# Kernel optimization log

Hardware: AMD Instinct MI355X
Metric: run time of the kernel (lower is better)

## Reference

```python
import jax, jax.numpy as jnp
import numpy as np

NQ = 10          # num_qubits
NL = 4           # num_layers (StronglyEntanglingLayers)
DIM = 2 ** NQ    # state-vector dimension = input_linear out features
B = 4096
SEQ = 512
PRED = 96

# ---- static basis-state bookkeeping (wire 0 = most significant bit, as in PennyLane) ----

def _cnot_perm(control, target):
    s = np.arange(DIM)
    bit = (s >> (NQ - 1 - control)) & 1
    return s ^ (bit << (NQ - 1 - target))

def _layer_perms():
    # StronglyEntanglingLayers default ranges: r_l = (l % (n_wires - 1)) + 1,
    # then CNOT(i, (i+r) % n) for i = 0..n-1, applied sequentially.
    perms = []
    for l in range(NL):
        r = (l % (NQ - 1)) + 1
        comp = np.arange(DIM)
        for c in range(NQ):
            g = _cnot_perm(c, (c + r) % NQ)
            comp = comp[g]          # compose: state_new[t] = state_old[comp[t]]
        perms.append(jnp.asarray(comp))
    return perms

PERMS = _layer_perms()

_bits = (np.arange(DIM)[:, None] >> (NQ - 1 - np.arange(NQ))[None, :]) & 1
SIGNS = jnp.asarray(1.0 - 2.0 * _bits, dtype=np.float32)   # [DIM, NQ] PauliZ eigenvalues


def _rot_gates(w):
    # PennyLane Rot(phi, theta, omega) = RZ(omega) @ RY(theta) @ RZ(phi); w: [L, n, 3]
    phi, theta, omega = w[..., 0], w[..., 1], w[..., 2]
    c = jnp.cos(theta / 2)
    s = jnp.sin(theta / 2)
    ep = jnp.exp(0.5j * (phi + omega))   # e^{+i(phi+omega)/2}
    em = jnp.exp(0.5j * (phi - omega))   # e^{+i(phi-omega)/2}
    m00 = jnp.conj(ep) * c
    m01 = -em * s
    m10 = jnp.conj(em) * s
    m11 = ep * c
    return jnp.stack([jnp.stack([m00, m01], -1),
                      jnp.stack([m10, m11], -1)], -2)       # [L, n, 2, 2] complex64


def _apply_1q(psi, U, wire):
    # psi: [B, DIM] complex; apply 2x2 U on `wire`
    b = psi.shape[0]
    left = 2 ** wire
    right = 2 ** (NQ - 1 - wire)
    psi = psi.reshape(b, left, 2, right)
    psi = jnp.einsum('ba,kpaq->kpbq', U, psi)
    return psi.reshape(b, DIM)


def _circuit(psi, q_weights):
    mats = _rot_gates(q_weights)
    for l in range(NL):
        for w in range(NQ):
            psi = _apply_1q(psi, mats[l, w], w)
        psi = psi[:, PERMS[l]]          # composed CNOT ring of this layer
    return psi


def reference(x, W_in, b_in, q_weights, W_out, b_out):
    h = x @ W_in.T + b_in + 1e-6                          # input_linear, then +1e-6
    norm = jnp.linalg.norm(h, axis=-1, keepdims=True)
    psi = (h / norm).astype(jnp.complex64)                # AmplitudeEmbedding(normalize=True)
    psi = _circuit(psi, q_weights)                        # StronglyEntanglingLayers
    probs = psi.real ** 2 + psi.imag ** 2
    expvals = probs @ SIGNS                               # [B, NQ] PauliZ expvals
    return expvals @ W_out.T + b_out                      # output_linear


def setup_inputs() -> dict:
    key = jax.random.key(0)
    ks = jax.random.split(key, 6)
    x = jax.random.normal(ks[0], (B, SEQ), dtype=jnp.float32)
    W_in = jax.random.normal(ks[1], (DIM, SEQ), dtype=jnp.float32) / np.sqrt(SEQ)
    b_in = jax.random.normal(ks[2], (DIM,), dtype=jnp.float32) * 0.01
    q_weights = jax.random.uniform(ks[3], (NL, NQ, 3), dtype=jnp.float32,
                                   minval=0.0, maxval=2.0 * np.pi)
    W_out = jax.random.normal(ks[4], (PRED, NQ), dtype=jnp.float32) / np.sqrt(NQ)
    b_out = jax.random.normal(ks[5], (PRED,), dtype=jnp.float32) * 0.01
    return {"x": x, "W_in": W_in, "b_in": b_in, "q_weights": q_weights,
            "W_out": W_out, "b_out": b_out}
```

## Files before the change

kernel.cpp:

```cpp
#include <hip/hip_runtime.h>
#include <math.h>

#define DIM 1024
#define NQ 10
#define NL 4
#define SEQ 512
#define NROWS 4096
#define PRED 96

typedef unsigned short ushort_t;
typedef unsigned int uint_t;
using half8   = __attribute__((ext_vector_type(8))) _Float16;
using float4v = __attribute__((ext_vector_type(4))) float;

__device__ inline ushort_t f2h(float f) { _Float16 h = (_Float16)f; return *(ushort_t*)&h; }
__device__ inline uint_t pkh(float a, float b) {
    _Float16 ha = (_Float16)a, hb = (_Float16)b;
    return (uint_t)(*(ushort_t*)&ha) | ((uint_t)(*(ushort_t*)&hb) << 16);
}

__global__ __launch_bounds__(512)
void circuit_cols_kernel(const float* __restrict__ Wi, const float* __restrict__ b_in,
                         const float* __restrict__ qw,
                         ushort_t* __restrict__ Crt_r, ushort_t* __restrict__ Crt_i,
                         float* __restrict__ dr, float* __restrict__ di)
{
    __shared__ float2 psi[DIM];
    __shared__ float gm[NL * NQ][8];

    const int tid = threadIdx.x;
    const int j = blockIdx.x;

    if (tid < NL * NQ) {
        float phi = qw[tid * 3 + 0], theta = qw[tid * 3 + 1], omega = qw[tid * 3 + 2];
        float ch = cosf(theta * 0.5f), sh = sinf(theta * 0.5f);
        float a = 0.5f * (phi + omega), b = 0.5f * (phi - omega);
        float ca = cosf(a), sa = sinf(a);
        float cb = cosf(b), sb = sinf(b);
        gm[tid][0] =  ch * ca;  gm[tid][1] = -ch * sa;
        gm[tid][2] = -sh * cb;  gm[tid][3] = -sh * sb;
        gm[tid][4] =  sh * cb;  gm[tid][5] = -sh * sb;
        gm[tid][6] =  ch * ca;  gm[tid][7] =  ch * sa;
    }

    float v0, v1;
    if (j < SEQ) {
        v0 = Wi[(size_t)(2 * tid) * SEQ + j];
        v1 = Wi[(size_t)(2 * tid + 1) * SEQ + j];
    } else {
        v0 = b_in[2 * tid] + 1e-6f;
        v1 = b_in[2 * tid + 1] + 1e-6f;
    }
    psi[2 * tid]     = make_float2(v0, 0.f);
    psi[2 * tid + 1] = make_float2(v1, 0.f);
    __syncthreads();

    for (int l = 0; l < NL; ++l) {
#pragma unroll
        for (int w = 0; w < NQ; ++w) {
            const float* m = gm[l * NQ + w];
            float m00r = m[0], m00i = m[1], m01r = m[2], m01i = m[3];
            float m10r = m[4], m10i = m[5], m11r = m[6], m11i = m[7];
            int mask = 1 << (9 - w);
            int lo = tid & (mask - 1);
            int s0 = ((tid ^ lo) << 1) | lo;
            int s1 = s0 | mask;
            float2 a0 = psi[s0], a1 = psi[s1];
            float2 n0, n1;
            n0.x = m00r * a0.x - m00i * a0.y + m01r * a1.x - m01i * a1.y;
            n0.y = m00r * a0.y + m00i * a0.x + m01r * a1.y + m01i * a1.x;
            n1.x = m10r * a0.x - m10i * a0.y + m11r * a1.x - m11i * a1.y;
            n1.y = m10r * a0.y + m10i * a0.x + m11r * a1.y + m11i * a1.x;
            psi[s0] = n0; psi[s1] = n1;
            __syncthreads();
        }
        int r = l % (NQ - 1) + 1;
        int p0 = tid, p1 = tid + 512;
#pragma unroll
        for (int c = 9; c >= 0; --c) {
            int t = (c + r) % NQ;
            p0 ^= ((p0 >> (9 - c)) & 1) << (9 - t);
            p1 ^= ((p1 >> (9 - c)) & 1) << (9 - t);
        }
        float2 t0 = psi[p0], t1 = psi[p1];
        __syncthreads();
        psi[tid] = t0; psi[tid + 512] = t1;
        __syncthreads();
    }

    float2 o0 = psi[tid], o1 = psi[tid + 512];
    if (j < SEQ) {
        Crt_r[(size_t)tid * SEQ + j]         = f2h(o0.x);
        Crt_i[(size_t)tid * SEQ + j]         = f2h(o0.y);
        Crt_r[(size_t)(tid + 512) * SEQ + j] = f2h(o1.x);
        Crt_i[(size_t)(tid + 512) * SEQ + j] = f2h(o1.y);
    } else {
        dr[tid] = o0.x;        di[tid] = o0.y;
        dr[tid + 512] = o1.x;  di[tid + 512] = o1.y;
    }
}

#define GBM 128
#define GBNC 64
#define GBK 32
#define LDA 40
#define LDP 65

__global__ __launch_bounds__(256)
void gemm_fused_kernel(const float* __restrict__ x,
                       const ushort_t* __restrict__ Crt_r, const ushort_t* __restrict__ Crt_i,
                       const float* __restrict__ dr, const float* __restrict__ di,
                       float* __restrict__ part)
{
    __shared__ __align__(16) char lds[GBM * LDP * 4];
    ushort_t* Ash = (ushort_t*)lds;
    ushort_t* Bsr = Ash + GBM * LDA;
    ushort_t* Bsi = Bsr + GBNC * LDA;
    float*    Ps  = (float*)lds;
    __shared__ float drs[GBNC], dis[GBNC];

    const int tid = threadIdx.x;
    const int bm = blockIdx.x, bn = blockIdx.y;
    const int lane = tid & 63, wv = tid >> 6;
    const int n0 = bn * GBNC;

    if (tid < GBNC) { drs[tid] = dr[n0 + tid]; dis[tid] = di[n0 + tid]; }

    float4v accr[2][4], acci[2][4];
#pragma unroll
    for (int a = 0; a < 2; ++a)
#pragma unroll
        for (int b = 0; b < 4; ++b) { accr[a][b] = (float4v)0.f; acci[a][b] = (float4v)0.f; }

    const int sr = tid >> 1, ko = (tid & 1) * 16;
    const float* xa = x + (size_t)(bm * GBM + sr) * SEQ + ko;
    const int bsel = tid >> 7;
    const int nr = (tid & 127) >> 1;
    const int bko = (tid & 1) * 16;
    const ushort_t* bsrc = (bsel ? Crt_i : Crt_r) + (size_t)(n0 + nr) * SEQ + bko;
    ushort_t* bdst = (bsel ? Bsi : Bsr) + nr * LDA + bko;

    const int fm = lane & 15, kq = (lane >> 4) * 8;
    const int wrow = wv * 32;

    for (int k0 = 0; k0 < SEQ; k0 += GBK) {
        float fv[16];
        *(float4*)&fv[0]  = *(const float4*)(xa + k0);
        *(float4*)&fv[4]  = *(const float4*)(xa + k0 + 4);
        *(float4*)&fv[8]  = *(const float4*)(xa + k0 + 8);
        *(float4*)&fv[12] = *(const float4*)(xa + k0 + 12);
        uint_t pk[8];
#pragma unroll
        for (int i = 0; i < 8; ++i) pk[i] = pkh(fv[2 * i], fv[2 * i + 1]);
        *(uint4*)(Ash + sr * LDA + ko)     = make_uint4(pk[0], pk[1], pk[2], pk[3]);
        *(uint4*)(Ash + sr * LDA + ko + 8) = make_uint4(pk[4], pk[5], pk[6], pk[7]);
        uint4 b0 = *(const uint4*)(bsrc + k0);
        uint4 b1 = *(const uint4*)(bsrc + k0 + 8);
        *(uint4*)bdst       = b0;
        *(uint4*)(bdst + 8) = b1;
        __syncthreads();

        half8 ah0 = *(half8*)(Ash + (wrow + fm) * LDA + kq);
        half8 ah1 = *(half8*)(Ash + (wrow + 16 + fm) * LDA + kq);
#pragma unroll
        for (int nt = 0; nt < 4; ++nt) {
            half8 br = *(half8*)(Bsr + (nt * 16 + fm) * LDA + kq);
            half8 bi = *(half8*)(Bsi + (nt * 16 + fm) * LDA + kq);
            accr[0][nt] = __builtin_amdgcn_mfma_f32_16x16x32_f16(ah0, br, accr[0][nt], 0, 0, 0);
            accr[1][nt] = __builtin_amdgcn_mfma_f32_16x16x32_f16(ah1, br, accr[1][nt], 0, 0, 0);
            acci[0][nt] = __builtin_amdgcn_mfma_f32_16x16x32_f16(ah0, bi, acci[0][nt], 0, 0, 0);
            acci[1][nt] = __builtin_amdgcn_mfma_f32_16x16x32_f16(ah1, bi, acci[1][nt], 0, 0, 0);
        }
        __syncthreads();
    }

    const int rq = (lane >> 4) * 4;
#pragma unroll
    for (int mt = 0; mt < 2; ++mt)
#pragma unroll
        for (int nt = 0; nt < 4; ++nt) {
            float drv = drs[nt * 16 + fm], div = dis[nt * 16 + fm];
#pragma unroll
            for (int reg = 0; reg < 4; ++reg) {
                int lrow = wrow + mt * 16 + rq + reg;
                float zr = accr[mt][nt][reg] + drv;
                float zi = acci[mt][nt][reg] + div;
                Ps[lrow * LDP + nt * 16 + fm] = zr * zr + zi * zi;
            }
        }
    __syncthreads();

    {
        const int row = tid >> 1, hh = tid & 1;
        const float* pr = Ps + row * LDP + hh * 32;
        float nrm = 0.f, e0 = 0.f, e1 = 0.f, e2 = 0.f, e3 = 0.f, e4 = 0.f, e5 = 0.f;
#pragma unroll
        for (int i = 0; i < 32; ++i) {
            float p = pr[i];
            int c = hh * 32 + i;
            nrm += p;
            e0 += ((c >> 5) & 1) ? -p : p;
            e1 += ((c >> 4) & 1) ? -p : p;
            e2 += ((c >> 3) & 1) ? -p : p;
            e3 += ((c >> 2) & 1) ? -p : p;
            e4 += ((c >> 1) & 1) ? -p : p;
            e5 += (c & 1) ? -p : p;
        }
        size_t base = ((size_t)(bm * GBM + row) * 32 + (bn * 2 + hh)) * 8;
        part[base + 0] = nrm;
        part[base + 1] = e0; part[base + 2] = e1; part[base + 3] = e2;
        part[base + 4] = e3; part[base + 5] = e4; part[base + 6] = e5;
    }
}

__global__ __launch_bounds__(128)
void finalize_kernel(const float* __restrict__ part, const float* __restrict__ W_out,
                     const float* __restrict__ b_out, float* __restrict__ out)
{
    __shared__ float evf[16];
    const int row = blockIdx.x, tid = threadIdx.x;

    if (tid < 64) {
        float v[11];
        if (tid < 32) {
            const float* p = part + ((size_t)row * 32 + tid) * 8;
            float4 a = *(const float4*)p;
            float4 b = *(const float4*)(p + 4);
            float nrm = a.x;
            int bnn = tid >> 1;
            v[0] = nrm;
            v[1] = (bnn & 8) ? -nrm : nrm;
            v[2] = (bnn & 4) ? -nrm : nrm;
            v[3] = (bnn & 2) ? -nrm : nrm;
            v[4] = (bnn & 1) ? -nrm : nrm;
            v[5] = a.y; v[6] = a.z; v[7] = a.w;
            v[8] = b.x; v[9] = b.y; v[10] = b.z;
        } else {
#pragma unroll
            for (int k = 0; k < 11; ++k) v[k] = 0.f;
        }
#pragma unroll
        for (int m = 16; m; m >>= 1)
#pragma unroll
            for (int k = 0; k < 11; ++k) v[k] += __shfl_xor(v[k], m, 64);
        if (tid == 0) {
            float inv = 1.0f / v[0];
#pragma unroll
            for (int k = 0; k < 10; ++k) evf[k] = v[k + 1] * inv;
        }
    }
    __syncthreads();
    if (tid < PRED) {
        float o = b_out[tid];
#pragma unroll
        for (int k = 0; k < NQ; ++k) o = fmaf(W_out[tid * NQ + k], evf[k], o);
        out[(size_t)row * PRED + tid] = o;
    }
}

extern "C" void kernel_launch(void* const* d_in, const int* in_sizes, int n_in,
                              void* d_out, int out_size, void* d_ws, size_t ws_size,
                              hipStream_t stream) {
    const float* x     = (const float*)d_in[0];
    const float* W_in  = (const float*)d_in[1];
    const float* b_in  = (const float*)d_in[2];
    const float* qw    = (const float*)d_in[3];
    const float* W_out = (const float*)d_in[4];
    const float* b_out = (const float*)d_in[5];
    float* out = (float*)d_out;

    char* w = (char*)d_ws;
    ushort_t* Crt_r = (ushort_t*)w;
    ushort_t* Crt_i = (ushort_t*)(w + (1u << 20));
    float* dr = (float*)(w + 2 * (1u << 20));
    float* di = dr + DIM;
    float* part = (float*)(w + 3 * (1u << 20));

    circuit_cols_kernel<<<SEQ + 1, 512, 0, stream>>>(W_in, b_in, qw, Crt_r, Crt_i, dr, di);
    dim3 g2(NROWS / GBM, DIM / GBNC);
    gemm_fused_kernel<<<g2, 256, 0, stream>>>(x, Crt_r, Crt_i, dr, di, part);
    finalize_kernel<<<NROWS, 128, 0, stream>>>(part, W_out, b_out, out);
}
```

Before: 114.7 us.

## Run circuit per wavefront in registers, pre-convert x to fp16, add transpose

```diff
diff --git a/kernel.cpp b/kernel.cpp
--- a/kernel.cpp
+++ b/kernel.cpp
@@ -13,23 +13,47 @@
 using half8   = __attribute__((ext_vector_type(8))) _Float16;
 using float4v = __attribute__((ext_vector_type(4))) float;
 
-__device__ inline ushort_t f2h(float f) { _Float16 h = (_Float16)f; return *(ushort_t*)&h; }
 __device__ inline uint_t pkh(float a, float b) {
     _Float16 ha = (_Float16)a, hb = (_Float16)b;
     return (uint_t)(*(ushort_t*)&ha) | ((uint_t)(*(ushort_t*)&hb) << 16);
 }
 
-__global__ __launch_bounds__(512)
-void circuit_cols_kernel(const float* __restrict__ Wi, const float* __restrict__ b_in,
+__device__ inline int permf(int s, int r) {
+#pragma unroll
+    for (int c = 9; c >= 0; --c) {
+        int t = (c + r) % 10;
+        s ^= ((s >> (9 - c)) & 1) << (9 - t);
+    }
+    return s;
+}
+
+__global__ __launch_bounds__(256)
+void convert_x_kernel(const float* __restrict__ x, ushort_t* __restrict__ xh)
+{
+    int i = (blockIdx.x * 256 + threadIdx.x) * 8;
+    float4 a = *(const float4*)(x + i);
+    float4 b = *(const float4*)(x + i + 4);
+    uint4 o;
+    o.x = pkh(a.x, a.y); o.y = pkh(a.z, a.w);
+    o.z = pkh(b.x, b.y); o.w = pkh(b.z, b.w);
+    *(uint4*)(xh + i) = o;
+}
+
+__global__ __launch_bounds__(256)
+void circuit_wave_kernel(const float* __restrict__ Wi, const float* __restrict__ b_in,
                          const float* __restrict__ qw,
-                         ushort_t* __restrict__ Crt_r, ushort_t* __restrict__ Crt_i,
+                         ushort_t* __restrict__ Cjm_r, ushort_t* __restrict__ Cjm_i,
                          float* __restrict__ dr, float* __restrict__ di)
 {
-    __shared__ float2 psi[DIM];
     __shared__ float gm[NL * NQ][8];
+    __shared__ float2 scr[4 * 1024];
 
     const int tid = threadIdx.x;
-    const int j = blockIdx.x;
+    const int lane = tid & 63;
+    const int wv = tid >> 6;
+    const int jorig = blockIdx.x * 4 + wv;
+    const bool valid = (jorig <= SEQ);
+    const int j = valid ? jorig : SEQ;
 
     if (tid < NL * NQ) {
         float phi = qw[tid * 3 + 0], theta = qw[tid * 3 + 1], omega = qw[tid * 3 + 2];
@@ -42,61 +66,124 @@
         gm[tid][4] =  sh * cb;  gm[tid][5] = -sh * sb;
         gm[tid][6] =  ch * ca;  gm[tid][7] =  ch * sa;
     }
-
-    float v0, v1;
+    __syncthreads();
+
+    float2 P[16];
     if (j < SEQ) {
-        v0 = Wi[(size_t)(2 * tid) * SEQ + j];
-        v1 = Wi[(size_t)(2 * tid + 1) * SEQ + j];
+#pragma unroll
+        for (int r = 0; r < 16; ++r)
+            P[r] = make_float2(Wi[(size_t)(lane * 16 + r) * SEQ + j], 0.f);
     } else {
-        v0 = b_in[2 * tid] + 1e-6f;
-        v1 = b_in[2 * tid + 1] + 1e-6f;
-    }
-    psi[2 * tid]     = make_float2(v0, 0.f);
-    psi[2 * tid + 1] = make_float2(v1, 0.f);
-    __syncthreads();
-
+#pragma unroll
+        for (int r = 0; r < 16; ++r)
+            P[r] = make_float2(b_in[lane * 16 + r] + 1e-6f, 0.f);
+    }
+
+    float2* wscr = scr + wv * 1024;
+
+#pragma unroll
     for (int l = 0; l < NL; ++l) {
 #pragma unroll
         for (int w = 0; w < NQ; ++w) {
             const float* m = gm[l * NQ + w];
             float m00r = m[0], m00i = m[1], m01r = m[2], m01i = m[3];
             float m10r = m[4], m10i = m[5], m11r = m[6], m11i = m[7];
-            int mask = 1 << (9 - w);
-            int lo = tid & (mask - 1);
-            int s0 = ((tid ^ lo) << 1) | lo;
-            int s1 = s0 | mask;
-            float2 a0 = psi[s0], a1 = psi[s1];
-            float2 n0, n1;
-            n0.x = m00r * a0.x - m00i * a0.y + m01r * a1.x - m01i * a1.y;
-            n0.y = m00r * a0.y + m00i * a0.x + m01r * a1.y + m01i * a1.x;
-            n1.x = m10r * a0.x - m10i * a0.y + m11r * a1.x - m11i * a1.y;
-            n1.y = m10r * a0.y + m10i * a0.x + m11r * a1.y + m11i * a1.x;
-            psi[s0] = n0; psi[s1] = n1;
-            __syncthreads();
-        }
-        int r = l % (NQ - 1) + 1;
-        int p0 = tid, p1 = tid + 512;
-#pragma unroll
-        for (int c = 9; c >= 0; --c) {
-            int t = (c + r) % NQ;
-            p0 ^= ((p0 >> (9 - c)) & 1) << (9 - t);
-            p1 ^= ((p1 >> (9 - c)) & 1) << (9 - t);
-        }
-        float2 t0 = psi[p0], t1 = psi[p1];
+            if (w <= 5) {
+                const int lb = 5 - w;
+                const int mask = 1 << lb;
+                const int myb = (lane >> lb) & 1;
+                float cAr = myb ? m11r : m00r, cAi = myb ? m11i : m00i;
+                float cQr = myb ? m10r : m01r, cQi = myb ? m10i : m01i;
+#pragma unroll
+                for (int r = 0; r < 16; ++r) {
+                    float ar = P[r].x, ai = P[r].y;
+                    float qr_ = __shfl_xor(ar, mask, 64);
+                    float qi_ = __shfl_xor(ai, mask, 64);
+                    P[r].x = cAr * ar - cAi * ai + cQr * qr_ - cQi * qi_;
+                    P[r].y = cAr * ai + cAi * ar + cQr * qi_ + cQi * qr_;
+                }
+            } else {
+                const int mk = 1 << (9 - w);
+#pragma unroll
+                for (int r0 = 0; r0 < 16; ++r0) {
+                    if (r0 & mk) continue;
+                    float2 a0 = P[r0], a1 = P[r0 | mk];
+                    float2 n0, n1;
+                    n0.x = m00r * a0.x - m00i * a0.y + m01r * a1.x - m01i * a1.y;
+                    n0.y = m00r * a0.y + m00i * a0.x + m01r * a1.y + m01i * a1.x;
+                    n1.x = m10r * a0.x - m10i * a0.y + m11r * a1.x - m11i * a1.y;
+                    n1.y = m10r * a0.y + m10i * a0.x + m11r * a1.y + m11i * a1.x;
+                    P[r0] = n0; P[r0 | mk] = n1;
+                }
+            }
+        }
+        const int rr = l % (NQ - 1) + 1;
+#pragma unroll
+        for (int r = 0; r < 16; ++r) wscr[lane * 16 + r] = P[r];
+        int pl = permf(lane << 4, rr);
+#pragma unroll
+        for (int r = 0; r < 16; ++r) {
+            int src = pl ^ permf(r, rr);
+            P[r] = wscr[src];
+        }
+    }
+
+    if (valid) {
+        if (j < SEQ) {
+            uint4 o0, o1, p0, p1;
+            o0.x = pkh(P[0].x,  P[1].x);  o0.y = pkh(P[2].x,  P[3].x);
+            o0.z = pkh(P[4].x,  P[5].x);  o0.w = pkh(P[6].x,  P[7].x);
+            o1.x = pkh(P[8].x,  P[9].x);  o1.y = pkh(P[10].x, P[11].x);
+            o1.z = pkh(P[12].x, P[13].x); o1.w = pkh(P[14].x, P[15].x);
+            p0.x = pkh(P[0].y,  P[1].y);  p0.y = pkh(P[2].y,  P[3].y);
+            p0.z = pkh(P[4].y,  P[5].y);  p0.w = pkh(P[6].y,  P[7].y);
+            p1.x = pkh(P[8].y,  P[9].y);  p1.y = pkh(P[10].y, P[11].y);
+            p1.z = pkh(P[12].y, P[13].y); p1.w = pkh(P[14].y, P[15].y);
+            size_t base = (size_t)j * DIM + lane * 16;
+            *(uint4*)(Cjm_r + base)     = o0;
+            *(uint4*)(Cjm_r + base + 8) = o1;
+            *(uint4*)(Cjm_i + base)     = p0;
+            *(uint4*)(Cjm_i + base + 8) = p1;
+        } else {
+#pragma unroll
+            for (int r = 0; r < 16; ++r) {
+                dr[lane * 16 + r] = P[r].x;
+                di[lane * 16 + r] = P[r].y;
+            }
+        }
+    }
+}
+
+__global__ __launch_bounds__(256)
+void transpose_c_kernel(const ushort_t* __restrict__ in_r, const ushort_t* __restrict__ in_i,
+                        ushort_t* __restrict__ out_r, ushort_t* __restrict__ out_i)
+{
+    __shared__ ushort_t Ts[64][80];
+    const int tid = threadIdx.x;
+    const int j0 = blockIdx.x * 64;
+    const int s0 = blockIdx.y * 64;
+
+    for (int a = 0; a < 2; ++a) {
+        const ushort_t* in = a ? in_i : in_r;
+        ushort_t* out = a ? out_i : out_r;
+#pragma unroll
+        for (int g = 0; g < 2; ++g) {
+            int G = tid + g * 256;
+            int jj = G >> 3, ch = G & 7;
+            uint4 v = *(const uint4*)(in + (size_t)(j0 + jj) * DIM + s0 + ch * 8);
+            const ushort_t* hv = (const ushort_t*)&v;
+#pragma unroll
+            for (int q = 0; q < 8; ++q) Ts[ch * 8 + q][jj] = hv[q];
+        }
         __syncthreads();
-        psi[tid] = t0; psi[tid + 512] = t1;
+#pragma unroll
+        for (int g = 0; g < 2; ++g) {
+            int G = tid + g * 256;
+            int ss = G >> 3, jc = G & 7;
+            uint4 v = *(const uint4*)(&Ts[ss][jc * 8]);
+            *(uint4*)(out + (size_t)(s0 + ss) * SEQ + j0 + jc * 8) = v;
+        }
         __syncthreads();
-    }
-
-    float2 o0 = psi[tid], o1 = psi[tid + 512];
-    if (j < SEQ) {
-        Crt_r[(size_t)tid * SEQ + j]         = f2h(o0.x);
-        Crt_i[(size_t)tid * SEQ + j]         = f2h(o0.y);
-        Crt_r[(size_t)(tid + 512) * SEQ + j] = f2h(o1.x);
-        Crt_i[(size_t)(tid + 512) * SEQ + j] = f2h(o1.y);
-    } else {
-        dr[tid] = o0.x;        di[tid] = o0.y;
-        dr[tid + 512] = o1.x;  di[tid + 512] = o1.y;
     }
 }
 
@@ -107,8 +194,8 @@
 #define LDP 65
 
 __global__ __launch_bounds__(256)
-void gemm_fused_kernel(const float* __restrict__ x,
-                       const ushort_t* __restrict__ Crt_r, const ushort_t* __restrict__ Crt_i,
+void gemm_fused_kernel(const ushort_t* __restrict__ xh,
+                       const ushort_t* __restrict__ Csm_r, const ushort_t* __restrict__ Csm_i,
                        const float* __restrict__ dr, const float* __restrict__ di,
                        float* __restrict__ part)
 {
@@ -133,27 +220,21 @@
         for (int b = 0; b < 4; ++b) { accr[a][b] = (float4v)0.f; acci[a][b] = (float4v)0.f; }
 
     const int sr = tid >> 1, ko = (tid & 1) * 16;
-    const float* xa = x + (size_t)(bm * GBM + sr) * SEQ + ko;
+    const ushort_t* xa = xh + (size_t)(bm * GBM + sr) * SEQ + ko;
     const int bsel = tid >> 7;
     const int nr = (tid & 127) >> 1;
     const int bko = (tid & 1) * 16;
-    const ushort_t* bsrc = (bsel ? Crt_i : Crt_r) + (size_t)(n0 + nr) * SEQ + bko;
+    const ushort_t* bsrc = (bsel ? Csm_i : Csm_r) + (size_t)(n0 + nr) * SEQ + bko;
     ushort_t* bdst = (bsel ? Bsi : Bsr) + nr * LDA + bko;
 
     const int fm = lane & 15, kq = (lane >> 4) * 8;
     const int wrow = wv * 32;
 
     for (int k0 = 0; k0 < SEQ; k0 += GBK) {
-        float fv[16];
-        *(float4*)&fv[0]  = *(const float4*)(xa + k0);
-        *(float4*)&fv[4]  = *(const float4*)(xa + k0 + 4);
-        *(float4*)&fv[8]  = *(const float4*)(xa + k0 + 8);
-        *(float4*)&fv[12] = *(const float4*)(xa + k0 + 12);
-        uint_t pk[8];
-#pragma unroll
-        for (int i = 0; i < 8; ++i) pk[i] = pkh(fv[2 * i], fv[2 * i + 1]);
-        *(uint4*)(Ash + sr * LDA + ko)     = make_uint4(pk[0], pk[1], pk[2], pk[3]);
-        *(uint4*)(Ash + sr * LDA + ko + 8) = make_uint4(pk[4], pk[5], pk[6], pk[7]);
+        uint4 a0 = *(const uint4*)(xa + k0);
+        uint4 a1 = *(const uint4*)(xa + k0 + 8);
+        *(uint4*)(Ash + sr * LDA + ko)     = a0;
+        *(uint4*)(Ash + sr * LDA + ko + 8) = a1;
         uint4 b0 = *(const uint4*)(bsrc + k0);
         uint4 b1 = *(const uint4*)(bsrc + k0 + 8);
         *(uint4*)bdst       = b0;
@@ -270,14 +351,20 @@
     float* out = (float*)d_out;
 
     char* w = (char*)d_ws;
-    ushort_t* Crt_r = (ushort_t*)w;
-    ushort_t* Crt_i = (ushort_t*)(w + (1u << 20));
-    float* dr = (float*)(w + 2 * (1u << 20));
-    float* di = dr + DIM;
-    float* part = (float*)(w + 3 * (1u << 20));
-
-    circuit_cols_kernel<<<SEQ + 1, 512, 0, stream>>>(W_in, b_in, qw, Crt_r, Crt_i, dr, di);
+    const size_t MB = 1u << 20;
+    ushort_t* xh    = (ushort_t*)w;
+    ushort_t* Cjm_r = (ushort_t*)(w + 4 * MB);
+    ushort_t* Cjm_i = (ushort_t*)(w + 5 * MB);
+    ushort_t* Csm_r = (ushort_t*)(w + 6 * MB);
+    ushort_t* Csm_i = (ushort_t*)(w + 7 * MB);
+    float*    dr    = (float*)(w + 8 * MB);
+    float*    di    = dr + DIM;
+    float*    part  = (float*)(w + 9 * MB);
+
+    convert_x_kernel<<<NROWS * SEQ / (256 * 8), 256, 0, stream>>>(x, xh);
+    circuit_wave_kernel<<<129, 256, 0, stream>>>(W_in, b_in, qw, Cjm_r, Cjm_i, dr, di);
+    transpose_c_kernel<<<dim3(SEQ / 64, DIM / 64), 256, 0, stream>>>(Cjm_r, Cjm_i, Csm_r, Csm_i);
     dim3 g2(NROWS / GBM, DIM / GBNC);
-    gemm_fused_kernel<<<g2, 256, 0, stream>>>(x, Crt_r, Crt_i, dr, di, part);
+    gemm_fused_kernel<<<g2, 256, 0, stream>>>(xh, Csm_r, Csm_i, dr, di, part);
     finalize_kernel<<<NROWS, 128, 0, stream>>>(part, W_out, b_out, out);
 }
```

Result: slower. 126.3 us (+10.2%).
